# Optimization experiments

Measured on AMD Instinct MI355X. Metric: run time of the kernel, lower is better.

The kernel has to match this reference:

```python
import jax, jax.numpy as jnp
import numpy as np

N = 100000   # nodes
E = 1600000  # edges
F = 256      # in/out feature dim
H = 64       # hidden dim


def _gcn_conv(x, edge_index, W, b):
    """PyG GCNConv: add self-loops, symmetric deg^-1/2 normalization, spmm, bias."""
    n = x.shape[0]
    loop = jnp.arange(n)
    src = jnp.concatenate([edge_index[0], loop])
    dst = jnp.concatenate([edge_index[1], loop])
    deg = jax.ops.segment_sum(jnp.ones(src.shape[0], dtype=x.dtype), dst, num_segments=n)
    dinv = jnp.where(deg > 0, deg ** -0.5, 0.0)
    norm = dinv[src] * dinv[dst]          # [E+N]
    h = x @ W                             # [N, out]
    out = jax.ops.segment_sum(h[src] * norm[:, None], dst, num_segments=n)
    return out + b


def _transformer_conv(x, edge_index, Wq, bq, Wk, bk, Wv, bv, Ws, bs):
    """PyG TransformerConv(heads=1): per-edge dot-product attention, softmax over
    incoming edges of each target node, weighted aggregate + root (skip) linear."""
    n = x.shape[0]
    src, dst = edge_index[0], edge_index[1]
    q = x @ Wq + bq
    k = x @ Wk + bk
    v = x @ Wv + bv
    scale = 1.0 / jnp.sqrt(jnp.asarray(q.shape[-1], x.dtype))
    logits = jnp.sum(q[dst] * k[src], axis=-1) * scale      # [E]
    m = jax.ops.segment_max(logits, dst, num_segments=n)
    m = jax.lax.stop_gradient(jnp.where(jnp.isfinite(m), m, 0.0))
    e = jnp.exp(logits - m[dst])                            # [E]
    denom = jax.ops.segment_sum(e, dst, num_segments=n)     # [N]
    agg = jax.ops.segment_sum(e[:, None] * v[src], dst, num_segments=n)  # [N, H]
    out = agg / jnp.where(denom > 0, denom, 1.0)[:, None]
    return out + x @ Ws + bs


def setup_inputs() -> dict:
    key = jax.random.key(0)
    ks = jax.random.split(key, 12)
    def lin(k, fan_in, fan_out):
        return jax.random.normal(k, (fan_in, fan_out), dtype=jnp.float32) / np.sqrt(fan_in)
    return {
        "x": jax.random.normal(ks[0], (N, F), dtype=jnp.float32),
        "edge_index": jax.random.randint(ks[1], (2, E), 0, N, dtype=jnp.int64),
        "W1": lin(ks[2], F, H), "b1": jnp.zeros((H,), jnp.float32),
        "Wq": lin(ks[3], H, H), "bq": jnp.zeros((H,), jnp.float32),
        "Wk": lin(ks[4], H, H), "bk": jnp.zeros((H,), jnp.float32),
        "Wv": lin(ks[5], H, H), "bv": jnp.zeros((H,), jnp.float32),
        "Ws": lin(ks[6], H, H), "bs": jnp.zeros((H,), jnp.float32),
        "W2": lin(ks[7], H, F), "b2": jnp.zeros((F,), jnp.float32),
    }


def reference(x, edge_index, W1, b1, Wq, bq, Wk, bk, Wv, bv, Ws, bs, W2, b2):
    h = _gcn_conv(x, edge_index, W1, b1)            # GCNConv(256 -> 64)
    h = jax.nn.relu(h)
    h = _transformer_conv(h, edge_index, Wq, bq, Wk, bk, Wv, bv, Ws, bs)  # TransformerConv(64->64)
    out = _gcn_conv(h, edge_index, W2, b2)          # GCNConv(64 -> 256)
    return out
```

## Files before the change

kernel.cpp:

```cpp
#include <hip/hip_runtime.h>
#include <hip/hip_bf16.h>

typedef unsigned short u16;
typedef unsigned int u32;

__device__ __forceinline__ float bl(u32 u) { union { u32 i; float f; } c; c.i = u << 16; return c.f; }
__device__ __forceinline__ float bh(u32 u) { union { u32 i; float f; } c; c.i = u & 0xffff0000u; return c.f; }
__device__ __forceinline__ u16 f2us(float f) {
    __hip_bfloat16 h = __float2bfloat16(f);
    return *reinterpret_cast<u16*>(&h);
}
__device__ __forceinline__ u32 pk2(float a, float b) {
    return (u32)f2us(a) | ((u32)f2us(b) << 16);
}
__device__ __forceinline__ void up8(uint4 u, float* f) {
    f[0] = bl(u.x); f[1] = bh(u.x); f[2] = bl(u.y); f[3] = bh(u.y);
    f[4] = bl(u.z); f[5] = bh(u.z); f[6] = bl(u.w); f[7] = bh(u.w);
}

typedef short bf16x8 __attribute__((ext_vector_type(8)));
typedef float f32x4 __attribute__((ext_vector_type(4)));

__global__ void k_hist(const int* __restrict__ dst, int* __restrict__ cnt, int E) {
    int e = blockIdx.x * 256 + threadIdx.x;
    if (e < E) atomicAdd(&cnt[dst[e]], 1);
}

__global__ void k_blocksum(const int* __restrict__ cnt, int* __restrict__ bsums, int n) {
    int base = blockIdx.x * 1024;
    int t = threadIdx.x;
    int s = 0;
    for (int j = t; j < 1024; j += 256) { int i = base + j; if (i < n) s += cnt[i]; }
    __shared__ int red[256];
    red[t] = s; __syncthreads();
    for (int off = 128; off > 0; off >>= 1) { if (t < off) red[t] += red[t + off]; __syncthreads(); }
    if (t == 0) bsums[blockIdx.x] = red[0];
}

__global__ void k_scan_bsums(int* __restrict__ bsums, int nb) {
    int t = threadIdx.x;
    int i0 = t * 4;
    int v[4]; int s = 0;
    #pragma unroll
    for (int j = 0; j < 4; j++) { v[j] = (i0 + j < nb) ? bsums[i0 + j] : 0; s += v[j]; }
    __shared__ int sc[256];
    sc[t] = s; __syncthreads();
    int acc = s;
    for (int off = 1; off < 256; off <<= 1) {
        int add = (t >= off) ? sc[t - off] : 0;
        __syncthreads();
        acc += add; sc[t] = acc;
        __syncthreads();
    }
    int run = acc - s;
    #pragma unroll
    for (int j = 0; j < 4; j++) {
        if (i0 + j < nb) { bsums[i0 + j] = run; run += v[j]; }
    }
}

__global__ void k_scan_final(int* __restrict__ cnt, const int* __restrict__ bsums,
                             int* __restrict__ rowptr, float* __restrict__ dinv, int n, int E) {
    int base = blockIdx.x * 1024;
    int t = threadIdx.x;
    int i0 = base + t * 4;
    int v[4]; int s = 0;
    for (int j = 0; j < 4; j++) { int i = i0 + j; v[j] = (i < n) ? cnt[i] : 0; s += v[j]; }
    __shared__ int sc[256];
    sc[t] = s; __syncthreads();
    int acc = s;
    for (int off = 1; off < 256; off <<= 1) {
        int add = (t >= off) ? sc[t - off] : 0;
        __syncthreads();
        acc += add; sc[t] = acc;
        __syncthreads();
    }
    int run = acc - s + bsums[blockIdx.x];
    for (int j = 0; j < 4; j++) {
        int i = i0 + j;
        if (i < n) {
            rowptr[i] = run;
            dinv[i] = rsqrtf((float)(v[j] + 1));
            cnt[i] = run;
            run += v[j];
        }
    }
    if (blockIdx.x == 0 && t == 0) rowptr[n] = E;
}

__global__ void k_scatter(const int* __restrict__ ei, int* __restrict__ cursor,
                          const float* __restrict__ dinv,
                          int2* __restrict__ edat, int E) {
    int e = blockIdx.x * 256 + threadIdx.x;
    if (e < E) {
        int s = ei[e], d = ei[E + e];
        int pos = atomicAdd(&cursor[d], 1);
        edat[pos] = make_int2(s, __float_as_int(dinv[s] * dinv[d]));
    }
}

__global__ void k_w2cast(const float* __restrict__ W2, u16* __restrict__ W2b) {
    int i = blockIdx.x * 256 + threadIdx.x;
    if (i < 64 * 256) W2b[i] = f2us(W2[i]);
}

__global__ void k_w1cast(const float* __restrict__ W1, u16* __restrict__ W1t) {
    int i = blockIdx.x * 256 + threadIdx.x;
    if (i < 64 * 256) {
        int col = i >> 8, k = i & 255;
        W1t[i] = f2us(W1[k * 64 + col]);
    }
}

__global__ void k_wcat(const float* __restrict__ Wq, const float* __restrict__ Wk,
                       const float* __restrict__ Wv, const float* __restrict__ Ws,
                       u16* __restrict__ Wcat) {
    int i = blockIdx.x * 256 + threadIdx.x;
    if (i < 256 * 64) {
        int col = i >> 6, k = i & 63;
        int m = col >> 6, mc = col & 63;
        const float* src = (m == 0) ? Wq : (m == 1) ? Wk : (m == 2) ? Wv : Ws;
        Wcat[i] = f2us(src[k * 64 + mc]);
    }
}

__global__ __launch_bounds__(256) void k_gemm1(const float* __restrict__ x,
                                               const u16* __restrict__ W1t,
                                               u16* __restrict__ xw1b, int n) {
    __shared__ u16 xs[16][264];
    int t = threadIdx.x, w = t >> 6, l = t & 63;
    int base = blockIdx.x * 16;
    int row = t >> 4, seg = t & 15;
    int node = base + row;
    const float4* src = (const float4*)(x + (size_t)(node < n ? node : n - 1) * 256 + seg * 16);
    float4 f0 = src[0], f1 = src[1], f2 = src[2], f3 = src[3];
    uint4 o0, o1;
    o0.x = pk2(f0.x, f0.y); o0.y = pk2(f0.z, f0.w);
    o0.z = pk2(f1.x, f1.y); o0.w = pk2(f1.z, f1.w);
    o1.x = pk2(f2.x, f2.y); o1.y = pk2(f2.z, f2.w);
    o1.z = pk2(f3.x, f3.y); o1.w = pk2(f3.z, f3.w);
    u16* dst = &xs[row][seg * 16];
    *(uint4*)dst = o0; *(uint4*)(dst + 8) = o1;
    __syncthreads();
    int c = l & 15, kg = l >> 4;
    int col = w * 16 + c;
    f32x4 acc = {0.f, 0.f, 0.f, 0.f};
    #pragma unroll
    for (int kk = 0; kk < 8; kk++) {
        bf16x8 a = *(const bf16x8*)&xs[c][kk * 32 + kg * 8];
        bf16x8 b = *(const bf16x8*)&W1t[(size_t)col * 256 + kk * 32 + kg * 8];
        acc = __builtin_amdgcn_mfma_f32_16x16x32_bf16(a, b, acc, 0, 0, 0);
    }
    #pragma unroll
    for (int r = 0; r < 4; r++) {
        int nd = base + kg * 4 + r;
        if (nd < n) xw1b[(size_t)nd * 64 + col] = f2us(acc[r]);
    }
}

__global__ __launch_bounds__(256) void k_agg1(const u16* __restrict__ xw1b,
                                              const int2* __restrict__ edat,
                                              const int* __restrict__ rowptr,
                                              const float* __restrict__ dinv,
                                              const float* __restrict__ b1,
                                              float* __restrict__ B, int n) {
    int t = threadIdx.x;
    int w = t >> 6, l = t & 63, g = l >> 3, li = l & 7;
    int node = blockIdx.x * 4 + w;
    if (node >= n) return;
    int beg = rowptr[node], end = rowptr[node + 1];
    float a0[8], a1[8];
    #pragma unroll
    for (int j = 0; j < 8; j++) { a0[j] = 0.f; a1[j] = 0.f; }
    for (int e0 = beg; e0 < end; e0 += 16) {
        int eA = e0 + g, eB = e0 + 8 + g;
        bool vA = (eA < end), vB = (eB < end);
        int2 dA = vA ? edat[eA] : make_int2(0, 0);
        int2 dB = vB ? edat[eB] : make_int2(0, 0);
        uint4 uA = *(const uint4*)(xw1b + (size_t)dA.x * 64 + li * 8);
        uint4 uB = *(const uint4*)(xw1b + (size_t)dB.x * 64 + li * 8);
        float wA = __int_as_float(dA.y), wB = __int_as_float(dB.y);
        float fA[8]; up8(uA, fA);
        float fB[8]; up8(uB, fB);
        #pragma unroll
        for (int j = 0; j < 8; j++) { a0[j] += fA[j] * wA; a1[j] += fB[j] * wB; }
    }
    #pragma unroll
    for (int j = 0; j < 8; j++) a0[j] += a1[j];
    #pragma unroll
    for (int off = 8; off <= 32; off <<= 1)
        #pragma unroll
        for (int j = 0; j < 8; j++) a0[j] += __shfl_xor(a0[j], off);
    if (g == 0) {
        float di = dinv[node], di2 = di * di;
        uint4 u = *(const uint4*)(xw1b + (size_t)node * 64 + li * 8);
        float sf[8]; up8(u, sf);
        float4 bv0 = *(const float4*)(b1 + li * 8);
        float4 bv1 = *(const float4*)(b1 + li * 8 + 4);
        float bb[8] = {bv0.x, bv0.y, bv0.z, bv0.w, bv1.x, bv1.y, bv1.z, bv1.w};
        float r[8];
        #pragma unroll
        for (int j = 0; j < 8; j++) r[j] = fmaxf(a0[j] + sf[j] * di2 + bb[j], 0.f);
        float* dst = B + (size_t)node * 64 + li * 8;
        *(float4*)dst = make_float4(r[0], r[1], r[2], r[3]);
        *(float4*)(dst + 4) = make_float4(r[4], r[5], r[6], r[7]);
    }
}

__global__ __launch_bounds__(256) void k_lin_qkvs(float* __restrict__ B,
                                                  const u16* __restrict__ Wcat,
                                                  const float* __restrict__ bq, const float* __restrict__ bk,
                                                  const float* __restrict__ bv, const float* __restrict__ bs,
                                                  u16* __restrict__ kvb, u16* __restrict__ h2b, int n) {
    __shared__ u16 hs[16][72];
    int t = threadIdx.x, w = t >> 6, l = t & 63;
    int base = blockIdx.x * 16;
    int row = t >> 4, q4 = t & 15;
    int node = base + row;
    if (node < n) {
        float4 f = *(const float4*)(B + (size_t)node * 64 + q4 * 4);
        uint2 o; o.x = pk2(f.x, f.y); o.y = pk2(f.z, f.w);
        *(uint2*)&hs[row][q4 * 4] = o;
    }
    __syncthreads();
    int c = l & 15, kg = l >> 4;
    bf16x8 a0 = *(const bf16x8*)&hs[c][kg * 8];
    bf16x8 a1 = *(const bf16x8*)&hs[c][32 + kg * 8];
    #pragma unroll
    for (int ti = 0; ti < 4; ti++) {
        int col = (w * 4 + ti) * 16 + c;
        bf16x8 b0 = *(const bf16x8*)&Wcat[(size_t)col * 64 + kg * 8];
        bf16x8 b1 = *(const bf16x8*)&Wcat[(size_t)col * 64 + 32 + kg * 8];
        f32x4 acc = {0.f, 0.f, 0.f, 0.f};
        acc = __builtin_amdgcn_mfma_f32_16x16x32_bf16(a0, b0, acc, 0, 0, 0);
        acc = __builtin_amdgcn_mfma_f32_16x16x32_bf16(a1, b1, acc, 0, 0, 0);
        int m = col >> 6, mc = col & 63;
        float bias = ((m == 0) ? bq : (m == 1) ? bk : (m == 2) ? bv : bs)[mc];
        #pragma unroll
        for (int r = 0; r < 4; r++) {
            int nd = base + kg * 4 + r;
            if (nd < n) {
                float v = acc[r] + bias;
                if (m == 0)      B[(size_t)nd * 64 + mc] = v;
                else if (m == 1) kvb[(size_t)nd * 128 + mc] = f2us(v);
                else if (m == 2) kvb[(size_t)nd * 128 + 64 + mc] = f2us(v);
                else             h2b[(size_t)nd * 64 + mc] = f2us(v);
            }
        }
    }
}

__global__ __launch_bounds__(256) void k_attn(const float* __restrict__ B,
                                              const u16* __restrict__ kvb,
                                              const int2* __restrict__ edat,
                                              const int* __restrict__ rowptr,
                                              u16* __restrict__ h2b, int n) {
    int t = threadIdx.x;
    int w = t >> 6, l = t & 63, g = l >> 3, li = l & 7;
    int node = blockIdx.x * 4 + w;
    if (node >= n) return;
    const float* qp = B + (size_t)node * 64 + li * 8;
    float4 qa = *(const float4*)qp;
    float4 qb = *(const float4*)(qp + 4);
    float q[8] = {qa.x, qa.y, qa.z, qa.w, qb.x, qb.y, qb.z, qb.w};
    int beg = rowptr[node], end = rowptr[node + 1];
    float mA = -1e30f, denA = 0.f, mB = -1e30f, denB = 0.f;
    float accA[8], accB[8];
    #pragma unroll
    for (int j = 0; j < 8; j++) { accA[j] = 0.f; accB[j] = 0.f; }
    for (int e0 = beg; e0 < end; e0 += 16) {
        int eA = e0 + g, eB = e0 + 8 + g;
        bool vA = (eA < end), vB = (eB < end);
        int sA = vA ? edat[eA].x : 0;
        int sB = vB ? edat[eB].x : 0;
        const u16* rowA = kvb + (size_t)sA * 128;
        const u16* rowB = kvb + (size_t)sB * 128;
        uint4 kuA = *(const uint4*)(rowA + li * 8);
        uint4 vuA = *(const uint4*)(rowA + 64 + li * 8);
        uint4 kuB = *(const uint4*)(rowB + li * 8);
        uint4 vuB = *(const uint4*)(rowB + 64 + li * 8);
        float kf[8], vf[8];
        up8(kuA, kf); up8(vuA, vf);
        float dA = 0.f;
        #pragma unroll
        for (int j = 0; j < 8; j++) dA += q[j] * kf[j];
        dA += __shfl_xor(dA, 1);
        dA += __shfl_xor(dA, 2);
        dA += __shfl_xor(dA, 4);
        float logitA = vA ? dA * 0.125f : -1e30f;
        float nmA = fmaxf(mA, logitA);
        float rA = __expf(mA - nmA);
        float pA = vA ? __expf(logitA - nmA) : 0.f;
        denA = denA * rA + pA;
        #pragma unroll
        for (int j = 0; j < 8; j++) accA[j] = accA[j] * rA + pA * vf[j];
        mA = nmA;
        up8(kuB, kf); up8(vuB, vf);
        float dB = 0.f;
        #pragma unroll
        for (int j = 0; j < 8; j++) dB += q[j] * kf[j];
        dB += __shfl_xor(dB, 1);
        dB += __shfl_xor(dB, 2);
        dB += __shfl_xor(dB, 4);
        float logitB = vB ? dB * 0.125f : -1e30f;
        float nmB = fmaxf(mB, logitB);
        float rB = __expf(mB - nmB);
        float pB = vB ? __expf(logitB - nmB) : 0.f;
        denB = denB * rB + pB;
        #pragma unroll
        for (int j = 0; j < 8; j++) accB[j] = accB[j] * rB + pB * vf[j];
        mB = nmB;
    }
    float m = fmaxf(mA, mB);
    float rA = __expf(mA - m), rB = __expf(mB - m);
    float den = denA * rA + denB * rB;
    float acc[8];
    #pragma unroll
    for (int j = 0; j < 8; j++) acc[j] = accA[j] * rA + accB[j] * rB;
    #pragma unroll
    for (int off = 8; off <= 32; off <<= 1) {
        float mo = __shfl_xor(m, off);
        float deno = __shfl_xor(den, off);
        float nm = fmaxf(m, mo);
        float r = __expf(m - nm), ro = __expf(mo - nm);
        den = den * r + deno * ro;
        #pragma unroll
        for (int j = 0; j < 8; j++) {
            float ao = __shfl_xor(acc[j], off);
            acc[j] = acc[j] * r + ao * ro;
        }
        m = nm;
    }
    if (g == 0) {
        float inv = (den > 0.f) ? 1.f / den : 0.f;
        u16* hp = h2b + (size_t)node * 64 + li * 8;
        uint4 su = *(const uint4*)hp;
        float sk[8]; up8(su, sk);
        float o[8];
        #pragma unroll
        for (int j = 0; j < 8; j++) o[j] = acc[j] * inv + sk[j];
        uint4 ou;
        ou.x = pk2(o[0], o[1]); ou.y = pk2(o[2], o[3]);
        ou.z = pk2(o[4], o[5]); ou.w = pk2(o[6], o[7]);
        *(uint4*)hp = ou;
    }
}

__global__ __launch_bounds__(256) void k_agg2gemm2(const u16* __restrict__ h2b,
                                                   const int2* __restrict__ edat,
                                                   const int* __restrict__ rowptr,
                                                   const float* __restrict__ dinv,
                                                   const u16* __restrict__ W2b,
                                                   const float* __restrict__ b2,
                                                   float* __restrict__ out, int n) {
    __shared__ u16 ag[16][72];
    int t = threadIdx.x, w = t >> 6, l = t & 63, g = l >> 3, li = l & 7;
    int base = blockIdx.x * 16;
    for (int i = w; i < 16; i += 4) {
        int node = base + i;
        float a0[8], a1[8];
        #pragma unroll
        for (int j = 0; j < 8; j++) { a0[j] = 0.f; a1[j] = 0.f; }
        if (node < n) {
            int beg = rowptr[node], end = rowptr[node + 1];
            for (int e0 = beg; e0 < end; e0 += 16) {
                int eA = e0 + g, eB = e0 + 8 + g;
                bool vA = (eA < end), vB = (eB < end);
                int2 dA = vA ? edat[eA] : make_int2(0, 0);
                int2 dB = vB ? edat[eB] : make_int2(0, 0);
                uint4 uA = *(const uint4*)(h2b + (size_t)dA.x * 64 + li * 8);
                uint4 uB = *(const uint4*)(h2b + (size_t)dB.x * 64 + li * 8);
                float wA = __int_as_float(dA.y), wB = __int_as_float(dB.y);
                float fA[8]; up8(uA, fA);
                float fB[8]; up8(uB, fB);
                #pragma unroll
                for (int j = 0; j < 8; j++) { a0[j] += fA[j] * wA; a1[j] += fB[j] * wB; }
            }
        }
        #pragma unroll
        for (int j = 0; j < 8; j++) a0[j] += a1[j];
        #pragma unroll
        for (int off = 8; off <= 32; off <<= 1)
            #pragma unroll
            for (int j = 0; j < 8; j++) a0[j] += __shfl_xor(a0[j], off);
        if (g == 0) {
            if (node < n) {
                float di = dinv[node], di2 = di * di;
                uint4 u = *(const uint4*)(h2b + (size_t)node * 64 + li * 8);
                float sf[8]; up8(u, sf);
                #pragma unroll
                for (int j = 0; j < 8; j++) a0[j] += sf[j] * di2;
            }
            uint4 ou;
            ou.x = pk2(a0[0], a0[1]); ou.y = pk2(a0[2], a0[3]);
            ou.z = pk2(a0[4], a0[5]); ou.w = pk2(a0[6], a0[7]);
            *(uint4*)&ag[i][li * 8] = ou;
        }
    }
    __syncthreads();
    int c = l & 15;
    int kg = l >> 4;
    bf16x8 alo = *(const bf16x8*)&ag[c][kg * 8];
    bf16x8 ahi = *(const bf16x8*)&ag[c][32 + kg * 8];
    #pragma unroll
    for (int ti = 0; ti < 4; ti++) {
        int ct = w * 4 + ti;
        int col = ct * 16 + c;
        bf16x8 blo, bhi;
        #pragma unroll
        for (int j = 0; j < 8; j++) {
            blo[j] = (short)W2b[(kg * 8 + j) * 256 + col];
            bhi[j] = (short)W2b[(32 + kg * 8 + j) * 256 + col];
        }
        f32x4 acc = {0.f, 0.f, 0.f, 0.f};
        acc = __builtin_amdgcn_mfma_f32_16x16x32_bf16(alo, blo, acc, 0, 0, 0);
        acc = __builtin_amdgcn_mfma_f32_16x16x32_bf16(ahi, bhi, acc, 0, 0, 0);
        float bias = b2[col];
        #pragma unroll
        for (int r = 0; r < 4; r++) {
            int node = base + kg * 4 + r;
            if (node < n) out[(size_t)node * 256 + col] = acc[r] + bias;
        }
    }
}

extern "C" void kernel_launch(void* const* d_in, const int* in_sizes, int n_in,
                              void* d_out, int out_size, void* d_ws, size_t ws_size,
                              hipStream_t stream) {
    const float* x  = (const float*)d_in[0];
    const int*   ei = (const int*)d_in[1];
    const float* W1 = (const float*)d_in[2];
    const float* b1 = (const float*)d_in[3];
    const float* Wq = (const float*)d_in[4];
    const float* bq = (const float*)d_in[5];
    const float* Wk = (const float*)d_in[6];
    const float* bk = (const float*)d_in[7];
    const float* Wv = (const float*)d_in[8];
    const float* bv = (const float*)d_in[9];
    const float* Ws = (const float*)d_in[10];
    const float* bs = (const float*)d_in[11];
    const float* W2 = (const float*)d_in[12];
    const float* b2 = (const float*)d_in[13];
    float* out = (float*)d_out;

    const int N = in_sizes[0] / 256;
    const int E = in_sizes[1] / 2;

    char* ob = (char*)d_out;
    u16*   kvb  = (u16*)ob;
    u16*   xw1b = (u16*)(ob + (size_t)N * 128 * 2);
    float* B    = (float*)(ob + (size_t)N * 128 * 2 + (size_t)N * 64 * 2);

    char* p = (char*)d_ws;
    auto alloc = [&](size_t bytes) { char* r = p; p += (bytes + 255) & ~(size_t)255; return r; };
    int*   cnt    = (int*)alloc((size_t)N * 4);
    int*   rowptr = (int*)alloc((size_t)(N + 1) * 4);
    int*   bsums  = (int*)alloc(4096);
    int2*  edat   = (int2*)alloc((size_t)E * 8);
    float* dinv   = (float*)alloc((size_t)N * 4);
    u16*   h2b    = (u16*)alloc((size_t)N * 64 * 2);
    u16*   W2b    = (u16*)alloc((size_t)64 * 256 * 2);
    u16*   W1t    = (u16*)alloc((size_t)64 * 256 * 2);
    u16*   Wcat   = (u16*)alloc((size_t)256 * 64 * 2);

    const int NB = (N + 1023) / 1024;

    hipMemsetAsync(cnt, 0, (size_t)N * 4, stream);
    k_hist<<<(E + 255) / 256, 256, 0, stream>>>(ei + E, cnt, E);
    k_blocksum<<<NB, 256, 0, stream>>>(cnt, bsums, N);
    k_scan_bsums<<<1, 256, 0, stream>>>(bsums, NB);
    k_scan_final<<<NB, 256, 0, stream>>>(cnt, bsums, rowptr, dinv, N, E);
    k_scatter<<<(E + 255) / 256, 256, 0, stream>>>(ei, cnt, dinv, edat, E);
    k_w2cast<<<64, 256, 0, stream>>>(W2, W2b);
    k_w1cast<<<64, 256, 0, stream>>>(W1, W1t);
    k_wcat<<<64, 256, 0, stream>>>(Wq, Wk, Wv, Ws, Wcat);

    k_gemm1<<<(N + 15) / 16, 256, 0, stream>>>(x, W1t, xw1b, N);
    k_agg1<<<(N + 3) / 4, 256, 0, stream>>>(xw1b, edat, rowptr, dinv, b1, B, N);
    k_lin_qkvs<<<(N + 15) / 16, 256, 0, stream>>>(B, Wcat, bq, bk, bv, bs, kvb, h2b, N);
    k_attn<<<(N + 3) / 4, 256, 0, stream>>>(B, kvb, edat, rowptr, h2b, N);
    k_agg2gemm2<<<(N + 15) / 16, 256, 0, stream>>>(h2b, edat, rowptr, dinv, W2b, b2, out, N);
}
```

Measured before the change: 432.7 us.

## Partition CSR scatter by XCD-owned destination ranges and fuse weight-cast kernels

The edge scatter now launches 8x512 blocks. Each group of blocks, chosen by blockIdx mod 8 to map onto one XCD, handles only edges whose destination lies in that XCD's eighth of the node range. This keeps the atomic cursors and edge writes local to one XCD's L2 and avoids cross-die contention. The cost is that every edge destination is read eight times. The three small weight-cast kernels are also merged into one launch to cut launch overhead.

```diff
diff --git a/kernel.cpp b/kernel.cpp
--- a/kernel.cpp
+++ b/kernel.cpp
@@ -90,37 +90,40 @@
 
 __global__ void k_scatter(const int* __restrict__ ei, int* __restrict__ cursor,
                           const float* __restrict__ dinv,
-                          int2* __restrict__ edat, int E) {
-    int e = blockIdx.x * 256 + threadIdx.x;
-    if (e < E) {
-        int s = ei[e], d = ei[E + e];
-        int pos = atomicAdd(&cursor[d], 1);
-        edat[pos] = make_int2(s, __float_as_int(dinv[s] * dinv[d]));
-    }
-}
-
-__global__ void k_w2cast(const float* __restrict__ W2, u16* __restrict__ W2b) {
+                          int2* __restrict__ edat, int E, int N) {
+    int xcd = blockIdx.x & 7;
+    int chunk = blockIdx.x >> 3;
+    int nchunks = gridDim.x >> 3;
+    int per = (E + nchunks - 1) / nchunks;
+    int beg = chunk * per;
+    int end = min(beg + per, E);
+    int lo = (int)(((long long)N * xcd) >> 3);
+    int hi = (int)(((long long)N * (xcd + 1)) >> 3);
+    for (int e = beg + (int)threadIdx.x; e < end; e += 256) {
+        int d = ei[E + e];
+        if (d >= lo && d < hi) {
+            int s = ei[e];
+            int pos = atomicAdd(&cursor[d], 1);
+            edat[pos] = make_int2(s, __float_as_int(dinv[s] * dinv[d]));
+        }
+    }
+}
+
+__global__ void k_wprep(const float* __restrict__ W1, const float* __restrict__ W2,
+                        const float* __restrict__ Wq, const float* __restrict__ Wk,
+                        const float* __restrict__ Wv, const float* __restrict__ Ws,
+                        u16* __restrict__ W1t, u16* __restrict__ W2b, u16* __restrict__ Wcat) {
     int i = blockIdx.x * 256 + threadIdx.x;
-    if (i < 64 * 256) W2b[i] = f2us(W2[i]);
-}
-
-__global__ void k_w1cast(const float* __restrict__ W1, u16* __restrict__ W1t) {
-    int i = blockIdx.x * 256 + threadIdx.x;
-    if (i < 64 * 256) {
-        int col = i >> 8, k = i & 255;
-        W1t[i] = f2us(W1[k * 64 + col]);
-    }
-}
-
-__global__ void k_wcat(const float* __restrict__ Wq, const float* __restrict__ Wk,
-                       const float* __restrict__ Wv, const float* __restrict__ Ws,
-                       u16* __restrict__ Wcat) {
-    int i = blockIdx.x * 256 + threadIdx.x;
-    if (i < 256 * 64) {
-        int col = i >> 6, k = i & 63;
+    if (i < 16384) {
+        W2b[i] = f2us(W2[i]);
+    } else if (i < 32768) {
+        int j = i - 16384; int col = j >> 8, k = j & 255;
+        W1t[j] = f2us(W1[k * 64 + col]);
+    } else if (i < 49152) {
+        int j = i - 32768; int col = j >> 6, k = j & 63;
         int m = col >> 6, mc = col & 63;
         const float* src = (m == 0) ? Wq : (m == 1) ? Wk : (m == 2) ? Wv : Ws;
-        Wcat[i] = f2us(src[k * 64 + mc]);
+        Wcat[j] = f2us(src[k * 64 + mc]);
     }
 }
 
@@ -470,10 +473,8 @@
     k_blocksum<<<NB, 256, 0, stream>>>(cnt, bsums, N);
     k_scan_bsums<<<1, 256, 0, stream>>>(bsums, NB);
     k_scan_final<<<NB, 256, 0, stream>>>(cnt, bsums, rowptr, dinv, N, E);
-    k_scatter<<<(E + 255) / 256, 256, 0, stream>>>(ei, cnt, dinv, edat, E);
-    k_w2cast<<<64, 256, 0, stream>>>(W2, W2b);
-    k_w1cast<<<64, 256, 0, stream>>>(W1, W1t);
-    k_wcat<<<64, 256, 0, stream>>>(Wq, Wk, Wv, Ws, Wcat);
+    k_scatter<<<512 * 8, 256, 0, stream>>>(ei, cnt, dinv, edat, E, N);
+    k_wprep<<<192, 256, 0, stream>>>(W1, W2, Wq, Wk, Wv, Ws, W1t, W2b, Wcat);
 
     k_gemm1<<<(N + 15) / 16, 256, 0, stream>>>(x, W1t, xw1b, N);
     k_agg1<<<(N + 3) / 4, 256, 0, stream>>>(xw1b, edat, rowptr, dinv, b1, B, N);
```

After: 423.3 us. 2.2% less time.
